# Kernel optimization log

Measured on AMD Instinct MI355X. Metric: run time of the kernel, lower is better.

## Reference

```python
import jax, jax.numpy as jnp
import numpy as np

C = 1.0          # curvature
MIN_NORM = 1e-15
EPS = 1e-7       # atanh clamp for fp32

def _sqnorm(x):
    return jnp.sum(x * x, axis=-1, keepdims=True)

def _norm(x):
    return jnp.sqrt(jnp.maximum(_sqnorm(x), MIN_NORM))

def _atanh(u):
    return jnp.arctanh(jnp.clip(u, -1.0 + EPS, 1.0 - EPS))

def mobius_add(x, y, c):
    x2 = _sqnorm(x); y2 = _sqnorm(y)
    xy = jnp.sum(x * y, axis=-1, keepdims=True)
    num = (1.0 + 2.0 * c * xy + c * y2) * x + (1.0 - c * x2) * y
    den = 1.0 + 2.0 * c * xy + c * c * x2 * y2
    return num / jnp.maximum(den, MIN_NORM)

def logmap0(p, c):
    sc = jnp.sqrt(c)
    pn = _norm(p)
    return p / pn / sc * _atanh(sc * pn)

def logmap(p1, p2, c):
    # tangent vector at p1 pointing to p2 (Poincare ball)
    sub = mobius_add(-p1, p2, c)
    sn = _norm(sub)
    lam = 2.0 / jnp.maximum(1.0 - c * _sqnorm(p1), MIN_NORM)
    sc = jnp.sqrt(c)
    return 2.0 / sc / lam * _atanh(sc * sn) * sub / sn

def expmap(p, u, c):
    un = _norm(u)
    lam = 2.0 / jnp.maximum(1.0 - c * _sqnorm(p), MIN_NORM)
    sc = jnp.sqrt(c)
    second = jnp.tanh(sc * lam * un / 2.0) * u / (sc * un)
    return mobius_add(p, second, c)


def setup_inputs() -> dict:
    key = jax.random.key(0)
    k1, k2, k3 = jax.random.split(key, 3)
    B, N, D = 1, 1024, 128
    # points inside the unit Poincare ball (||x|| ~ 0.23)
    x = jax.random.normal(k1, (B, N, D), jnp.float32) * 0.02
    # sparse-ish dense adjacency mask (0/1 floats)
    adj = (jax.random.uniform(k2, (B, N, N)) < 0.05).astype(jnp.float32)
    # DenseAtt: nn.Linear(2*D, 1) weight (flattened) + bias
    att_w = jax.random.normal(k3, (2 * D,), jnp.float32) * 0.1
    att_b = jnp.zeros((), jnp.float32)
    return {"x": x, "adj": adj, "att_w": att_w, "att_b": att_b}


def reference(x, adj, att_w, att_b):
    B, N, D = x.shape
    x_t = logmap0(x, C)                                   # [B,N,D]
    # DenseAtt: sigmoid(Linear(cat(x_i, x_j))) decomposed as left_i + right_j + b
    left = x_t @ att_w[:D]                                # [B,N]
    right = x_t @ att_w[D:]                               # [B,N]
    att = jax.nn.sigmoid(left[:, :, None] + right[:, None, :] + att_b) * adj  # [B,N,N]
    # pairwise logmap: tangent at x_i of every x_j  -> [B,N,N,D]
    x_local = logmap(x[:, :, None, :], x[:, None, :, :], C)
    support_t = jnp.einsum('bij,bijd->bid', att, x_local)  # [B,N,D]
    return expmap(x, support_t, C)
```

## Files before the change

kernel.cpp:

```cpp
#include <hip/hip_runtime.h>
#include <math.h>


typedef short short8v __attribute__((ext_vector_type(8)));
typedef float float4v __attribute__((ext_vector_type(4)));

static __device__ __forceinline__ short f2bf(float f) {
    unsigned u = __float_as_uint(f);
    u += 0x7fff + ((u >> 16) & 1);
    return (short)(u >> 16);
}
static __device__ __forceinline__ float rcpf(float x) { return __builtin_amdgcn_rcpf(x); }
static __device__ __forceinline__ float atanh_over(float pn) {
    float uu = fminf(pn, 1.f - 1e-7f);
    return 0.5f * __logf((1.f + uu) * rcpf(1.f - uu)) * rcpf(pn);
}
static __device__ __forceinline__ void gload16(const unsigned short* g, unsigned short* l) {
    __builtin_amdgcn_global_load_lds(
        (const __attribute__((address_space(1))) void*)g,
        (__attribute__((address_space(3))) void*)l, 16, 0, 0);
}

__global__ __launch_bounds__(256) void hyp_stats(
    const float* __restrict__ x, const float* __restrict__ w,
    const float* __restrict__ battp,
    float* __restrict__ st_x2, float* __restrict__ st_L, float* __restrict__ st_R,
    unsigned short* __restrict__ xb, unsigned short* __restrict__ xbT)
{
    int row  = blockIdx.x * 4 + (threadIdx.x >> 6);
    int lane = threadIdx.x & 63;
    const float* xr = x + row * 128;
    float a0 = xr[lane], a1 = xr[lane + 64];

    unsigned short b0 = (unsigned short)f2bf(a0);
    unsigned short b1 = (unsigned short)f2bf(a1);
    int r7 = row & 7, l7 = lane & 7;
    xb[row * 128 + ((lane >> 3) ^ r7) * 8 + l7]        = b0;
    xb[row * 128 + (((lane + 64) >> 3) ^ r7) * 8 + l7] = b1;
    int tb = (row >> 7) * 128 + (row & 7);
    int uo = (row & 127) >> 3;
    xbT[lane * 1024        + tb + (uo ^ l7) * 8] = b0;
    xbT[(lane + 64) * 1024 + tb + (uo ^ l7) * 8] = b1;

    float x2 = a0 * a0 + a1 * a1;
    float dl = a0 * w[lane]       + a1 * w[lane + 64];
    float dr = a0 * w[lane + 128] + a1 * w[lane + 192];
    for (int m = 1; m < 64; m <<= 1) {
        x2 += __shfl_xor(x2, m);
        dl += __shfl_xor(dl, m);
        dr += __shfl_xor(dr, m);
    }
    if (lane == 0) {
        float pn = sqrtf(fmaxf(x2, 1e-15f));
        float f  = atanh_over(pn);
        st_x2[row] = x2;
        st_L[row]  = f * dl + battp[0];
        st_R[row]  = f * dr;
    }
}

__global__ __launch_bounds__(256, 2) void hyp_main(
    const float* __restrict__ adj,
    const float* __restrict__ st_x2, const float* __restrict__ st_L,
    const float* __restrict__ st_R,
    const unsigned short* __restrict__ xb, const unsigned short* __restrict__ xbT,
    float* __restrict__ Yp, float* __restrict__ Sp)
{
    __shared__ __align__(16) unsigned short sXI [16 * 128];
    __shared__ __align__(16) unsigned short sXJ [128 * 128];
    __shared__ __align__(16) unsigned short sXJt[128 * 128];
    __shared__ __align__(16) unsigned short sW  [16 * 128];

    const int t    = threadIdx.x;
    const int lane = t & 63;
    const int wave = t >> 6;
    const int n    = lane & 15;
    const int q    = lane >> 4;
    const int i0   = blockIdx.x * 16;
    const int c    = blockIdx.y;
    const int j0   = c * 128;

    gload16(&xb[i0 * 128 + t * 8], &sXI[wave * 512]);
#pragma unroll
    for (int it = 0; it < 8; ++it)
        gload16(&xb[j0 * 128 + (it * 256 + t) * 8], &sXJ[(it * 256 + wave * 64) * 8]);
#pragma unroll
    for (int it = 0; it < 8; ++it) {
        int s = it * 256 + t;
        gload16(&xbT[(s >> 4) * 1024 + j0 + (s & 15) * 8],
                &sXJt[(it * 256 + wave * 64) * 8]);
    }

    float x2i4[4], bi4[4], li4[4];
#pragma unroll
    for (int r = 0; r < 4; ++r) {
        int i = i0 + q * 4 + r;
        x2i4[r] = st_x2[i];
        li4[r]  = st_L[i];
    }
    float x2j2[2], rj2[2], adjv[2][4];
#pragma unroll
    for (int jsl = 0; jsl < 2; ++jsl) {
        int j = j0 + (wave * 2 + jsl) * 16 + n;
        x2j2[jsl] = st_x2[j];
        rj2[jsl]  = st_R[j];
#pragma unroll
        for (int r = 0; r < 4; ++r)
            adjv[jsl][r] = adj[(i0 + q * 4 + r) * 1024 + j];
    }
#pragma unroll
    for (int r = 0; r < 4; ++r) bi4[r] = 1.f - x2i4[r];

    __syncthreads();

    const int n7 = n & 7;
    short8v afrag[4];
#pragma unroll
    for (int kk = 0; kk < 4; ++kk)
        afrag[kk] = *(const short8v*)&sXI[(n * 16 + ((kk * 4 + q) ^ n7)) * 8];

    float Sacc[4] = {0.f, 0.f, 0.f, 0.f};

#pragma unroll
    for (int jsl = 0; jsl < 2; ++jsl) {
        int js = wave * 2 + jsl;
        int jrow = js * 16 + n;
        float4v acc = (float4v){0.f, 0.f, 0.f, 0.f};
#pragma unroll
        for (int kk = 0; kk < 4; ++kk) {
            short8v b = *(const short8v*)&sXJ[(jrow * 16 + ((kk * 4 + q) ^ n7)) * 8];
            acc = __builtin_amdgcn_mfma_f32_16x16x32_bf16(afrag[kk], b, acc, 0, 0, 0);
        }
        float x2j = x2j2[jsl];
        float rj  = rj2[jsl];
#pragma unroll
        for (int r = 0; r < 4; ++r) {
            float G     = acc[r];
            int   i     = q * 4 + r;
            float alpha = 1.f - 2.f * G + x2j;
            float den   = fmaxf(fmaf(x2i4[r], x2j, 1.f - 2.f * G), 1e-15f);
            float rdn   = rcpf(den);
            float bb    = bi4[r];
            float nn2   = alpha * alpha * x2i4[r] + bb * bb * x2j - 2.f * alpha * bb * G;
            float sn    = sqrtf(fmaxf(nn2 * rdn * rdn, 1e-15f));
            float tt    = atanh_over(sn);
            float z     = li4[r] + rj;
            float sig   = rcpf(1.f + __expf(-z));
            float g     = sig * adjv[jsl][r] * tt * rdn;
            Sacc[r]     = fmaf(g, alpha, Sacc[r]);
            sW[(i * 16 + ((js * 2 + (n >> 3)) ^ (i & 7))) * 8 + n7] = (unsigned short)f2bf(g);
        }
    }
    __syncthreads();

    float4v accB[2];
    accB[0] = (float4v){0.f, 0.f, 0.f, 0.f};
    accB[1] = (float4v){0.f, 0.f, 0.f, 0.f};
#pragma unroll
    for (int nsl = 0; nsl < 2; ++nsl) {
        int ns = wave * 2 + nsl;
#pragma unroll
        for (int kk = 0; kk < 4; ++kk) {
            short8v a = *(const short8v*)&sW  [(n * 16 + ((kk * 4 + q) ^ n7)) * 8];
            short8v b = *(const short8v*)&sXJt[((ns * 16 + n) * 16 + ((kk * 4 + q) ^ n7)) * 8];
            accB[nsl] = __builtin_amdgcn_mfma_f32_16x16x32_bf16(a, b, accB[nsl], 0, 0, 0);
        }
    }

    float* Yc = Yp + c * 131072;
#pragma unroll
    for (int nsl = 0; nsl < 2; ++nsl) {
        int ns = wave * 2 + nsl;
#pragma unroll
        for (int r = 0; r < 4; ++r)
            Yc[(i0 + q * 4 + r) * 128 + ns * 16 + n] = accB[nsl][r];
    }
#pragma unroll
    for (int r = 0; r < 4; ++r) {
#pragma unroll
        for (int m = 1; m < 16; m <<= 1)
            Sacc[r] += __shfl_xor(Sacc[r], m);
    }
    if (n == 0) {
#pragma unroll
        for (int r = 0; r < 4; ++r)
            Sp[(c * 1024 + i0 + q * 4 + r) * 4 + wave] = Sacc[r];
    }
}

__global__ __launch_bounds__(256) void hyp_exp(
    const float* __restrict__ x, const float* __restrict__ Yp,
    const float* __restrict__ Sp, const float* __restrict__ st_x2,
    float* __restrict__ out)
{
    const int t   = threadIdx.x;
    const int row = blockIdx.x * 8 + (t >> 5);
    const int l32 = t & 31;
    float4v y = (float4v){0.f, 0.f, 0.f, 0.f};
#pragma unroll
    for (int c = 0; c < 8; ++c)
        y += *(const float4v*)&Yp[c * 131072 + row * 128 + l32 * 4];
    float S = Sp[((l32 >> 2) * 1024 + row) * 4 + (l32 & 3)];
#pragma unroll
    for (int m = 1; m < 32; m <<= 1) S += __shfl_xor(S, m, 32);

    float4v xa = ((const float4v*)x)[row * 32 + l32];
    float x2 = st_x2[row];
    float bE = fmaxf(1.f - x2, 1e-15f);
    float u[4], un2p = 0.f, xup = 0.f;
#pragma unroll
    for (int e = 0; e < 4; ++e) {
        u[e] = bE * (bE * y[e] - S * xa[e]);
        un2p += u[e] * u[e];
        xup  += xa[e] * u[e];
    }
#pragma unroll
    for (int m = 1; m < 32; m <<= 1) {
        un2p += __shfl_xor(un2p, m, 32);
        xup  += __shfl_xor(xup,  m, 32);
    }
    float un  = sqrtf(fmaxf(un2p, 1e-15f));
    float e2  = __expf(2.f * un * rcpf(bE));
    float th  = 1.f - 2.f * rcpf(e2 + 1.f);
    float s2  = th * rcpf(un);
    float xy  = s2 * xup;
    float y2s = th * th;
    float coef = 1.f + 2.f * xy + y2s;
    float den  = fmaxf(1.f + 2.f * xy + x2 * y2s, 1e-15f);
    float rd   = rcpf(den);
    float4v o = { (coef*xa[0] + bE*s2*u[0])*rd, (coef*xa[1] + bE*s2*u[1])*rd,
                  (coef*xa[2] + bE*s2*u[2])*rd, (coef*xa[3] + bE*s2*u[3])*rd };
    ((float4v*)out)[row * 32 + l32] = o;
}

extern "C" void kernel_launch(void* const* d_in, const int* in_sizes, int n_in,
                              void* d_out, int out_size, void* d_ws, size_t ws_size,
                              hipStream_t stream) {
    const float* x    = (const float*)d_in[0];
    const float* adj  = (const float*)d_in[1];
    const float* w    = (const float*)d_in[2];
    const float* batt = (const float*)d_in[3];
    float* out = (float*)d_out;

    float* Yp    = (float*)d_ws;
    float* Sp    = Yp + 8 * 131072;
    float* st_x2 = Sp + 8 * 1024 * 4;
    float* st_L  = st_x2 + 1024;
    float* st_R  = st_L + 1024;
    unsigned short* xb  = (unsigned short*)(st_R + 1024);
    unsigned short* xbT = xb + 1024 * 128;

    hipLaunchKernelGGL(hyp_stats, dim3(256), dim3(256), 0, stream,
                       x, w, batt, st_x2, st_L, st_R, xb, xbT);
    hipLaunchKernelGGL(hyp_main, dim3(64, 8), dim3(256), 0, stream,
                       adj, st_x2, st_L, st_R, xb, xbT, Yp, Sp);
    hipLaunchKernelGGL(hyp_exp, dim3(128), dim3(256), 0, stream,
                       x, Yp, Sp, st_x2, out);
}
```

Baseline: 72.68 us.

## Fuse expmap epilogue into main kernel via last-block atomic ticket

Removes the separate hyp_exp launch. Each row-block of hyp_main bumps a per-row-tile atomic ticket, and the eighth (last) column block to finish reduces the partial Y and S sums and applies expmap directly. Tickets are zeroed in hyp_stats and reset after use. This saves one kernel launch and its gap, at the cost of an atomic, extra barriers and a serialized tail in the last block for each row tile.

```diff
diff --git a/kernel.cpp b/kernel.cpp
--- a/kernel.cpp
+++ b/kernel.cpp
@@ -25,8 +25,11 @@
     const float* __restrict__ x, const float* __restrict__ w,
     const float* __restrict__ battp,
     float* __restrict__ st_x2, float* __restrict__ st_L, float* __restrict__ st_R,
-    unsigned short* __restrict__ xb, unsigned short* __restrict__ xbT)
+    unsigned short* __restrict__ xb, unsigned short* __restrict__ xbT,
+    unsigned* __restrict__ tickets)
 {
+    if (blockIdx.x == 0 && threadIdx.x < 64) tickets[threadIdx.x] = 0u;
+
     int row  = blockIdx.x * 4 + (threadIdx.x >> 6);
     int lane = threadIdx.x & 63;
     const float* xr = x + row * 128;
@@ -60,16 +63,18 @@
 }
 
 __global__ __launch_bounds__(256, 2) void hyp_main(
-    const float* __restrict__ adj,
+    const float* __restrict__ x, const float* __restrict__ adj,
     const float* __restrict__ st_x2, const float* __restrict__ st_L,
     const float* __restrict__ st_R,
     const unsigned short* __restrict__ xb, const unsigned short* __restrict__ xbT,
-    float* __restrict__ Yp, float* __restrict__ Sp)
+    float* __restrict__ Yp, float* __restrict__ Sp,
+    unsigned* __restrict__ tickets, float* __restrict__ out)
 {
     __shared__ __align__(16) unsigned short sXI [16 * 128];
     __shared__ __align__(16) unsigned short sXJ [128 * 128];
     __shared__ __align__(16) unsigned short sXJt[128 * 128];
     __shared__ __align__(16) unsigned short sW  [16 * 128];
+    __shared__ int sdone;
 
     const int t    = threadIdx.x;
     const int lane = t & 63;
@@ -186,38 +191,50 @@
         for (int r = 0; r < 4; ++r)
             Sp[(c * 1024 + i0 + q * 4 + r) * 4 + wave] = Sacc[r];
     }
-}
-
-__global__ __launch_bounds__(256) void hyp_exp(
-    const float* __restrict__ x, const float* __restrict__ Yp,
-    const float* __restrict__ Sp, const float* __restrict__ st_x2,
-    float* __restrict__ out)
-{
-    const int t   = threadIdx.x;
-    const int row = blockIdx.x * 8 + (t >> 5);
-    const int l32 = t & 31;
-    float4v y = (float4v){0.f, 0.f, 0.f, 0.f};
-#pragma unroll
-    for (int c = 0; c < 8; ++c)
-        y += *(const float4v*)&Yp[c * 131072 + row * 128 + l32 * 4];
-    float S = Sp[((l32 >> 2) * 1024 + row) * 4 + (l32 & 3)];
-#pragma unroll
-    for (int m = 1; m < 32; m <<= 1) S += __shfl_xor(S, m, 32);
-
-    float4v xa = ((const float4v*)x)[row * 32 + l32];
+
+    __syncthreads();
+    if (t == 0) {
+        unsigned old = __hip_atomic_fetch_add(&tickets[blockIdx.x], 1u,
+                          __ATOMIC_ACQ_REL, __HIP_MEMORY_SCOPE_AGENT);
+        sdone = (old == 7u);
+    }
+    __syncthreads();
+    if (!sdone) return;
+    __builtin_amdgcn_fence(__ATOMIC_ACQUIRE, "agent");
+
+    const int rl  = t >> 4;
+    const int row = i0 + rl;
+    const int l16 = t & 15;
+    float4v y0 = (float4v){0.f, 0.f, 0.f, 0.f};
+    float4v y1 = (float4v){0.f, 0.f, 0.f, 0.f};
+#pragma unroll
+    for (int cc = 0; cc < 8; ++cc) {
+        const float4v* Yr = (const float4v*)&Yp[cc * 131072 + row * 128];
+        y0 += Yr[l16 * 2];
+        y1 += Yr[l16 * 2 + 1];
+    }
+    float S = Sp[((l16 >> 2) * 1024 + row) * 4 + (l16 & 3)]
+            + Sp[(((l16 + 16) >> 2) * 1024 + row) * 4 + ((l16 + 16) & 3)];
+#pragma unroll
+    for (int m = 1; m < 16; m <<= 1) S += __shfl_xor(S, m);
+
+    const float4v* x4g = (const float4v*)x;
+    float4v xa0 = x4g[row * 32 + l16 * 2];
+    float4v xa1 = x4g[row * 32 + l16 * 2 + 1];
     float x2 = st_x2[row];
     float bE = fmaxf(1.f - x2, 1e-15f);
-    float u[4], un2p = 0.f, xup = 0.f;
+    float u0[4], u1[4], un2p = 0.f, xup = 0.f;
 #pragma unroll
     for (int e = 0; e < 4; ++e) {
-        u[e] = bE * (bE * y[e] - S * xa[e]);
-        un2p += u[e] * u[e];
-        xup  += xa[e] * u[e];
-    }
-#pragma unroll
-    for (int m = 1; m < 32; m <<= 1) {
-        un2p += __shfl_xor(un2p, m, 32);
-        xup  += __shfl_xor(xup,  m, 32);
+        u0[e] = bE * (bE * y0[e] - S * xa0[e]);
+        u1[e] = bE * (bE * y1[e] - S * xa1[e]);
+        un2p += u0[e] * u0[e] + u1[e] * u1[e];
+        xup  += xa0[e] * u0[e] + xa1[e] * u1[e];
+    }
+#pragma unroll
+    for (int m = 1; m < 16; m <<= 1) {
+        un2p += __shfl_xor(un2p, m);
+        xup  += __shfl_xor(xup,  m);
     }
     float un  = sqrtf(fmaxf(un2p, 1e-15f));
     float e2  = __expf(2.f * un * rcpf(bE));
@@ -228,9 +245,16 @@
     float coef = 1.f + 2.f * xy + y2s;
     float den  = fmaxf(1.f + 2.f * xy + x2 * y2s, 1e-15f);
     float rd   = rcpf(den);
-    float4v o = { (coef*xa[0] + bE*s2*u[0])*rd, (coef*xa[1] + bE*s2*u[1])*rd,
-                  (coef*xa[2] + bE*s2*u[2])*rd, (coef*xa[3] + bE*s2*u[3])*rd };
-    ((float4v*)out)[row * 32 + l32] = o;
+    float4v o0 = { (coef*xa0[0] + bE*s2*u0[0])*rd, (coef*xa0[1] + bE*s2*u0[1])*rd,
+                   (coef*xa0[2] + bE*s2*u0[2])*rd, (coef*xa0[3] + bE*s2*u0[3])*rd };
+    float4v o1 = { (coef*xa1[0] + bE*s2*u1[0])*rd, (coef*xa1[1] + bE*s2*u1[1])*rd,
+                   (coef*xa1[2] + bE*s2*u1[2])*rd, (coef*xa1[3] + bE*s2*u1[3])*rd };
+    ((float4v*)out)[row * 32 + l16 * 2]     = o0;
+    ((float4v*)out)[row * 32 + l16 * 2 + 1] = o1;
+
+    if (t == 0)
+        __hip_atomic_store(&tickets[blockIdx.x], 0u,
+                           __ATOMIC_RELEASE, __HIP_MEMORY_SCOPE_AGENT);
 }
 
 extern "C" void kernel_launch(void* const* d_in, const int* in_sizes, int n_in,
@@ -249,11 +273,10 @@
     float* st_R  = st_L + 1024;
     unsigned short* xb  = (unsigned short*)(st_R + 1024);
     unsigned short* xbT = xb + 1024 * 128;
+    unsigned* tickets   = (unsigned*)(xbT + 1024 * 128);
 
     hipLaunchKernelGGL(hyp_stats, dim3(256), dim3(256), 0, stream,
-                       x, w, batt, st_x2, st_L, st_R, xb, xbT);
+                       x, w, batt, st_x2, st_L, st_R, xb, xbT, tickets);
     hipLaunchKernelGGL(hyp_main, dim3(64, 8), dim3(256), 0, stream,
-                       adj, st_x2, st_L, st_R, xb, xbT, Yp, Sp);
-    hipLaunchKernelGGL(hyp_exp, dim3(128), dim3(256), 0, stream,
-                       x, Yp, Sp, st_x2, out);
-}
+                       x, adj, st_x2, st_L, st_R, xb, xbT, Yp, Sp, tickets, out);
+}
```

New measurement: 90.73 us. 1.25x slower.
